# Optimization experiments

Measured on AMD Instinct MI355X. Metric: run time of the kernel, lower is better.

Reference implementation:

```python
import jax, jax.numpy as jnp
import numpy as np

B, S, HID = 4, 2048, 1024
NH = 16
HD = HID // NH  # 64


def setup_inputs() -> dict:
    key = jax.random.key(0)
    k1, k2, k3 = jax.random.split(key, 3)
    x = jax.random.normal(k1, (B, S, HID), dtype=jnp.float32)
    # causal sparse mask: True = attend
    mask = jnp.tril(jnp.ones((S, S), dtype=bool))
    w_qkv = jax.random.normal(k2, (HID, 3 * HID), dtype=jnp.float32) * 0.02
    b_qkv = jnp.zeros((3 * HID,), dtype=jnp.float32)
    w_out = jax.random.normal(k3, (HID, HID), dtype=jnp.float32) * 0.02
    b_out = jnp.zeros((HID,), dtype=jnp.float32)
    return {"x": x, "mask": mask, "w_qkv": w_qkv, "b_qkv": b_qkv,
            "w_out": w_out, "b_out": b_out}


def reference(x, mask, w_qkv, b_qkv, w_out, b_out):
    bsz, seq_len, hid = x.shape
    # QKV projection -> [B, S, H, 3*D] -> [B, H, S, 3*D]
    qkv = (x @ w_qkv + b_qkv).reshape(bsz, seq_len, NH, 3 * HD).transpose(0, 2, 1, 3)
    q, k, v = jnp.split(qkv, 3, axis=-1)  # each [B, H, S, D]
    scale = 1.0 / jnp.sqrt(jnp.asarray(HD, dtype=x.dtype))
    scores = jnp.einsum('bhqd,bhkd->bhqk', q, k) * scale
    scores = jnp.where(mask[None, None, :, :], scores, jnp.asarray(-jnp.inf, dtype=scores.dtype))
    probs = jax.nn.softmax(scores, axis=-1)
    context = jnp.einsum('bhqk,bhkd->bhqd', probs, v)  # [B, H, S, D]
    context = context.transpose(0, 2, 1, 3).reshape(bsz, seq_len, hid)
    return context @ w_out + b_out
```

## Files before the change

kernel.cpp:

```cpp
#include <hip/hip_runtime.h>
#include <stdint.h>

#define S_LEN 2048
#define NHEAD 16
#define HDIM  64
#define HIDDEN 1024
#define BATCH 4

typedef float f32x4 __attribute__((ext_vector_type(4)));
typedef __bf16 bf16x8 __attribute__((ext_vector_type(8)));
typedef unsigned short u16;

union U4B8 { uint4 u; bf16x8 b; };

__device__ __forceinline__ bf16x8 as_b8(uint4 u){ U4B8 x; x.u = u; return x.b; }

__device__ __forceinline__ f32x4 mfma16(uint4 a, uint4 b, f32x4 c){
  return __builtin_amdgcn_mfma_f32_16x16x32_bf16(as_b8(a), as_b8(b), c, 0, 0, 0);
}

__device__ __forceinline__ u16 f2bf(float f){
  __bf16 h = (__bf16)f;
  return __builtin_bit_cast(u16, h);
}

__device__ __forceinline__ float exp2fast(float x){
  return __builtin_exp2f(x);
}

__device__ __forceinline__ void gload16(const void* g, void* l){
  __builtin_amdgcn_global_load_lds(
      (const __attribute__((address_space(1))) unsigned int*)g,
      (__attribute__((address_space(3))) unsigned int*)l, 16, 0, 0);
}

#define QSCALE 0.18033688f
#define DEFER_THR 11.5f

__global__ __launch_bounds__(256) void k_cvt(const float* __restrict__ in,
                                             u16* __restrict__ out, int n4){
  int i = blockIdx.x * 256 + threadIdx.x;
  int stride = gridDim.x * 256;
  for (; i < n4; i += stride){
    float4 v = ((const float4*)in)[i];
    unsigned lo = (unsigned)f2bf(v.x) | ((unsigned)f2bf(v.y) << 16);
    unsigned hi = (unsigned)f2bf(v.z) | ((unsigned)f2bf(v.w) << 16);
    ((uint2*)out)[i] = make_uint2(lo, hi);
  }
}

__global__ __launch_bounds__(256) void k_transpose(const float* __restrict__ in,
                                                   u16* __restrict__ out,
                                                   int K, int N){
  __shared__ float t[32][33];
  int tx = threadIdx.x & 31, ty = threadIdx.x >> 5;
  int n0 = blockIdx.x * 32, k0 = blockIdx.y * 32;
  #pragma unroll
  for (int i = 0; i < 4; ++i)
    t[ty + i*8][tx] = in[(size_t)(k0 + ty + i*8) * N + n0 + tx];
  __syncthreads();
  #pragma unroll
  for (int i = 0; i < 4; ++i)
    out[(size_t)(n0 + ty + i*8) * K + k0 + tx] = f2bf(t[tx][ty + i*8]);
}

__device__ __forceinline__ void stage_gemm(
    const u16* __restrict__ A, const u16* __restrict__ Bt,
    u16* As, u16* Bs, int row0, int col0, int K, int k0, int wave, int lane)
{
  #pragma unroll
  for (int p = 0; p < 2; ++p){
    int chunk = wave * 128 + p * 64 + lane;
    int r = chunk >> 2, cseg = chunk & 3;
    const u16* ga = A  + (size_t)(row0 + r) * K + k0 + cseg * 8;
    gload16(ga, As + (size_t)(wave * 128 + p * 64) * 8);
    const u16* gb = Bt + (size_t)(col0 + r) * K + k0 + cseg * 8;
    gload16(gb, Bs + (size_t)(wave * 128 + p * 64) * 8);
  }
}

template<int MODE>
__global__ __launch_bounds__(256) void k_gemm(
    const u16* __restrict__ A, const u16* __restrict__ Bt,
    const float* __restrict__ bias,
    u16* __restrict__ oq, u16* __restrict__ ok, u16* __restrict__ ov,
    float* __restrict__ of, int M, int N, int K)
{
  __shared__ u16 As[2][128 * 32];
  __shared__ u16 Bs[2][128 * 32];
  const int tid  = threadIdx.x;
  const int wave = tid >> 6, lane = tid & 63;
  const int l4 = lane >> 4, lm = lane & 15;
  const int wr = wave >> 1, wc = wave & 1;
  const int row0 = blockIdx.y * 128;
  const int col0 = blockIdx.x * 128;

  const f32x4 fzero = {0.f, 0.f, 0.f, 0.f};
  f32x4 acc[4][4];
  #pragma unroll
  for (int m = 0; m < 4; ++m)
    #pragma unroll
    for (int n = 0; n < 4; ++n) acc[m][n] = fzero;

  stage_gemm(A, Bt, &As[0][0], &Bs[0][0], row0, col0, K, 0, wave, lane);

  const int nks = K >> 5;
  #pragma unroll 1
  for (int ks = 0; ks < nks; ++ks){
    const int cur = ks & 1;
    if (ks + 1 < nks){
      stage_gemm(A, Bt, &As[cur ^ 1][0], &Bs[cur ^ 1][0],
                 row0, col0, K, (ks + 1) << 5, wave, lane);
      asm volatile("s_waitcnt vmcnt(4)" ::: "memory");
    } else {
      asm volatile("s_waitcnt vmcnt(0)" ::: "memory");
    }
    __builtin_amdgcn_s_barrier();
    asm volatile("" ::: "memory");

    uint4 af[4], bf[4];
    #pragma unroll
    for (int m = 0; m < 4; ++m)
      af[m] = *(const uint4*)&As[cur][(wr * 64 + m * 16 + lm) * 32 + l4 * 8];
    #pragma unroll
    for (int n = 0; n < 4; ++n)
      bf[n] = *(const uint4*)&Bs[cur][(wc * 64 + n * 16 + lm) * 32 + l4 * 8];
    __builtin_amdgcn_s_setprio(1);
    #pragma unroll
    for (int m = 0; m < 4; ++m)
      #pragma unroll
      for (int n = 0; n < 4; ++n)
        acc[m][n] = mfma16(af[m], bf[n], acc[m][n]);
    __builtin_amdgcn_s_setprio(0);

    asm volatile("" ::: "memory");
    __builtin_amdgcn_s_barrier();
    asm volatile("" ::: "memory");
  }

  #pragma unroll
  for (int m = 0; m < 4; ++m){
    #pragma unroll
    for (int n = 0; n < 4; ++n){
      int c = col0 + wc * 64 + n * 16 + lm;
      float bv = bias[c];
      #pragma unroll
      for (int r = 0; r < 4; ++r){
        int row = row0 + wr * 64 + m * 16 + l4 * 4 + r;
        float val = acc[m][n][r] + bv;
        if (MODE == 0){
          int h = c / 192, e = c % 192;
          int which = e >> 6, d = e & 63;
          int b = row >> 11, s = row & 2047;
          int bh = b * 16 + h;
          if (which == 2){
            ov[((size_t)bh * HDIM + d) * S_LEN + s] = f2bf(val);
          } else {
            if (which == 0) val *= QSCALE;
            size_t idx = ((size_t)bh * S_LEN + s) * HDIM + d;
            u16* dst = (which == 0) ? oq : ok;
            dst[idx] = f2bf(val);
          }
        } else {
          of[(size_t)row * N + c] = val;
        }
      }
    }
  }
}

__device__ __forceinline__ void stage_tile(
    const u16* __restrict__ kB, const u16* __restrict__ vB,
    u16* ldsK, u16* ldsV, int kbase, int wave, int lane)
{
  #pragma unroll
  for (int p = 0; p < 2; ++p){
    int ch  = wave * 128 + p * 64 + lane;
    int row = ch >> 3;
    int cc  = (ch & 7) << 4;
    int sc  = cc ^ ((row & 7) << 4);
    const u16* gk = kB + (size_t)(kbase + row) * HDIM + (sc >> 1);
    gload16(gk, ldsK + (size_t)(wave * 128 + p * 64) * 8);
    const u16* gv = vB + (size_t)row * S_LEN + kbase + (sc >> 1);
    gload16(gv, ldsV + (size_t)(wave * 128 + p * 64) * 8);
  }
}

__global__ __launch_bounds__(256) void k_attn(
    const u16* __restrict__ q, const u16* __restrict__ kk,
    const u16* __restrict__ vt, u16* __restrict__ ctx)
{
  __shared__ u16 KV[2][2][64 * 64];
  __shared__ u16 Ps[4][2][16][72];

  const int bid = blockIdx.x;
  const int bh = bid & 63;
  const int pr = bid >> 6;
  const int wave = threadIdx.x >> 6, lane = threadIdx.x & 63;
  const int l4 = lane >> 4, lm = lane & 15;
  const size_t base = (size_t)bh * (S_LEN * HDIM);
  const u16* kB = kk + base;
  const u16* vB = vt + base;
  const int b = bh >> 4, h = bh & 15;
  const f32x4 fz = {0.f, 0.f, 0.f, 0.f};

  #pragma unroll 1
  for (int half = 0; half < 2; ++half){
    const int st = half ? (15 - pr) : pr;
    const int q0 = st * 128 + wave * 32;

    uint4 qf[2][2];
    #pragma unroll
    for (int f = 0; f < 2; ++f){
      const u16* qr = q + base + (size_t)(q0 + f * 16 + lm) * HDIM + l4 * 8;
      qf[f][0] = *(const uint4*)qr;
      qf[f][1] = *(const uint4*)(qr + 32);
    }

    float mr[2] = {-1e30f, -1e30f}, lsp[2] = {0.f, 0.f};
    f32x4 acc[2][4];
    #pragma unroll
    for (int f = 0; f < 2; ++f)
      #pragma unroll
      for (int tt = 0; tt < 4; ++tt) acc[f][tt] = fz;

    const int nkt = 2 * st + 2;

    stage_tile(kB, vB, &KV[0][0][0], &KV[0][1][0], 0, wave, lane);

    #pragma unroll 1
    for (int kt = 0; kt < nkt; ++kt){
      const int cur = kt & 1;
      const int kbase = kt << 6;
      if (kt + 1 < nkt){
        stage_tile(kB, vB, &KV[cur ^ 1][0][0], &KV[cur ^ 1][1][0],
                   (kt + 1) << 6, wave, lane);
        asm volatile("s_waitcnt vmcnt(4)" ::: "memory");
      } else {
        asm volatile("s_waitcnt vmcnt(0)" ::: "memory");
      }
      __builtin_amdgcn_s_barrier();
      asm volatile("" ::: "memory");

      if (kbase < q0 + 32){
        const u16* ldsK = &KV[cur][0][0];
        const u16* ldsV = &KV[cur][1][0];

        f32x4 sv[2][4];
        __builtin_amdgcn_s_setprio(1);
        #pragma unroll
        for (int g = 0; g < 4; ++g){
          int rk = g * 16 + lm;
          int xa = (l4 * 16) ^ ((rk & 7) << 4);
          int xb = (64 + l4 * 16) ^ ((rk & 7) << 4);
          const u16* krow = ldsK + rk * 64;
          uint4 kf0 = *(const uint4*)(krow + (xa >> 1));
          uint4 kf1 = *(const uint4*)(krow + (xb >> 1));
          sv[0][g] = mfma16(kf0, qf[0][0], fz);
          sv[0][g] = mfma16(kf1, qf[0][1], sv[0][g]);
          sv[1][g] = mfma16(kf0, qf[1][0], fz);
          sv[1][g] = mfma16(kf1, qf[1][1], sv[1][g]);
        }
        __builtin_amdgcn_s_setprio(0);

        const bool tail = (kbase + 63 > q0);

        #pragma unroll
        for (int f = 0; f < 2; ++f){
          if (tail){
            #pragma unroll
            for (int g = 0; g < 4; ++g)
              #pragma unroll
              for (int r = 0; r < 4; ++r){
                int kg = kbase + g * 16 + l4 * 4 + r;
                int qg = q0 + f * 16 + lm;
                if (kg > qg) sv[f][g][r] = -1e30f;
              }
          }

          float pm = sv[f][0][0];
          #pragma unroll
          for (int g = 0; g < 4; ++g)
            #pragma unroll
            for (int r = 0; r < 4; ++r) pm = fmaxf(pm, sv[f][g][r]);
          pm = fmaxf(pm, __shfl_xor(pm, 16));
          pm = fmaxf(pm, __shfl_xor(pm, 32));

          if (__any(pm > mr[f] + DEFER_THR)){
            float mn = fmaxf(mr[f], pm);
            float corr = exp2fast(mr[f] - mn);
            mr[f] = mn;
            lsp[f] *= corr;
            float cf[4];
            #pragma unroll
            for (int r = 0; r < 4; ++r) cf[r] = __shfl(corr, l4 * 4 + r);
            #pragma unroll
            for (int tt = 0; tt < 4; ++tt)
              #pragma unroll
              for (int r = 0; r < 4; ++r) acc[f][tt][r] *= cf[r];
          }

          float s_ = 0.f;
          #pragma unroll
          for (int g = 0; g < 4; ++g){
            float p0 = exp2fast(sv[f][g][0] - mr[f]);
            float p1 = exp2fast(sv[f][g][1] - mr[f]);
            float p2 = exp2fast(sv[f][g][2] - mr[f]);
            float p3 = exp2fast(sv[f][g][3] - mr[f]);
            s_ += (p0 + p1) + (p2 + p3);
            uint2 w;
            w.x = (unsigned)f2bf(p0) | ((unsigned)f2bf(p1) << 16);
            w.y = (unsigned)f2bf(p2) | ((unsigned)f2bf(p3) << 16);
            *(uint2*)&Ps[wave][f][lm][g * 16 + l4 * 4] = w;
          }
          lsp[f] += s_;
        }

        __builtin_amdgcn_wave_barrier();
        uint4 pa[2][2];
        #pragma unroll
        for (int f = 0; f < 2; ++f){
          pa[f][0] = *(const uint4*)&Ps[wave][f][lm][l4 * 8];
          pa[f][1] = *(const uint4*)&Ps[wave][f][lm][32 + l4 * 8];
        }

        __builtin_amdgcn_s_setprio(1);
        #pragma unroll
        for (int tt = 0; tt < 4; ++tt){
          int rv = tt * 16 + lm;
          int xa = (l4 * 16) ^ ((rv & 7) << 4);
          int xb = (64 + l4 * 16) ^ ((rv & 7) << 4);
          const u16* vrow = ldsV + rv * 64;
          uint4 v0 = *(const uint4*)(vrow + (xa >> 1));
          uint4 v1 = *(const uint4*)(vrow + (xb >> 1));
          acc[0][tt] = mfma16(pa[0][0], v0, acc[0][tt]);
          acc[0][tt] = mfma16(pa[0][1], v1, acc[0][tt]);
          acc[1][tt] = mfma16(pa[1][0], v0, acc[1][tt]);
          acc[1][tt] = mfma16(pa[1][1], v1, acc[1][tt]);
        }
        __builtin_amdgcn_s_setprio(0);
      }

      asm volatile("" ::: "memory");
      __builtin_amdgcn_s_barrier();
      asm volatile("" ::: "memory");
    }

    #pragma unroll
    for (int f = 0; f < 2; ++f){
      lsp[f] += __shfl_xor(lsp[f], 16);
      lsp[f] += __shfl_xor(lsp[f], 32);
      float inv_ = 1.0f / lsp[f];
      float ivr[4];
      #pragma unroll
      for (int r = 0; r < 4; ++r) ivr[r] = __shfl(inv_, l4 * 4 + r);
      #pragma unroll
      for (int tt = 0; tt < 4; ++tt)
        #pragma unroll
        for (int r = 0; r < 4; ++r){
          int srow = q0 + f * 16 + l4 * 4 + r;
          float val = acc[f][tt][r] * ivr[r];
          ctx[((size_t)b * S_LEN + srow) * HIDDEN + h * HDIM + tt * 16 + lm] = f2bf(val);
        }
    }
  }
}

extern "C" void kernel_launch(void* const* d_in, const int* in_sizes, int n_in,
                              void* d_out, int out_size, void* d_ws, size_t ws_size,
                              hipStream_t stream)
{
  const float* x     = (const float*)d_in[0];
  const float* w_qkv = (const float*)d_in[2];
  const float* b_qkv = (const float*)d_in[3];
  const float* w_out = (const float*)d_in[4];
  const float* b_out = (const float*)d_in[5];

  char* ws = (char*)d_ws;
  u16* xbf   = (u16*)(ws);
  u16* wqkvT = (u16*)(ws + 16777216);
  u16* woutT = (u16*)(ws + 23068672);
  u16* qb    = (u16*)(ws + 25165824);
  u16* kb    = (u16*)(ws + 41943040);
  u16* vb    = (u16*)(ws + 58720256);

  k_cvt<<<2048, 256, 0, stream>>>(x, xbf, (BATCH * S_LEN * HIDDEN) / 4);
  k_transpose<<<dim3(96, 32), 256, 0, stream>>>(w_qkv, wqkvT, HIDDEN, 3 * HIDDEN);
  k_transpose<<<dim3(32, 32), 256, 0, stream>>>(w_out, woutT, HIDDEN, HIDDEN);
  k_gemm<0><<<dim3(24, 64), 256, 0, stream>>>(xbf, wqkvT, b_qkv,
                                              qb, kb, vb, nullptr,
                                              BATCH * S_LEN, 3 * HIDDEN, HIDDEN);
  k_attn<<<512, 256, 0, stream>>>(qb, kb, vb, xbf);
  k_gemm<1><<<dim3(8, 64), 256, 0, stream>>>(xbf, woutT, b_out,
                                             nullptr, nullptr, nullptr,
                                             (float*)d_out, BATCH * S_LEN, HIDDEN, HIDDEN);
}
```

Baseline: 218.3 us.

## Split attention query tile across eight waves with 16 rows each

The attention kernel now launches 512 threads per block (8 waves), each wave owning 16 query rows instead of 32, and the K/V staging is split so each wave loads one chunk per tile. This raises the number of waves available to hide latency and lowers per-wave register pressure, and the causal skip becomes finer-grained per wave. In exchange each K/V fragment read from LDS now feeds half as many MFMAs, so LDS traffic per FLOP doubles, and block-wide barriers now synchronise twice as many waves.

Measured after the change: 201.3 us. 1.08x faster.

```diff
diff --git a/kernel.cpp b/kernel.cpp
--- a/kernel.cpp
+++ b/kernel.cpp
@@ -169,29 +169,24 @@
   }
 }
 
-__device__ __forceinline__ void stage_tile(
+__device__ __forceinline__ void stage_tile8(
     const u16* __restrict__ kB, const u16* __restrict__ vB,
     u16* ldsK, u16* ldsV, int kbase, int wave, int lane)
 {
-  #pragma unroll
-  for (int p = 0; p < 2; ++p){
-    int ch  = wave * 128 + p * 64 + lane;
-    int row = ch >> 3;
-    int cc  = (ch & 7) << 4;
-    int sc  = cc ^ ((row & 7) << 4);
-    const u16* gk = kB + (size_t)(kbase + row) * HDIM + (sc >> 1);
-    gload16(gk, ldsK + (size_t)(wave * 128 + p * 64) * 8);
-    const u16* gv = vB + (size_t)row * S_LEN + kbase + (sc >> 1);
-    gload16(gv, ldsV + (size_t)(wave * 128 + p * 64) * 8);
-  }
-}
-
-__global__ __launch_bounds__(256) void k_attn(
+  int ch  = wave * 64 + lane;
+  int row = ch >> 3;
+  int cc  = (ch & 7) << 4;
+  int sc  = cc ^ ((row & 7) << 4);
+  gload16(kB + (size_t)(kbase + row) * HDIM + (sc >> 1), ldsK + (size_t)wave * 512);
+  gload16(vB + (size_t)row * S_LEN + kbase + (sc >> 1), ldsV + (size_t)wave * 512);
+}
+
+__global__ __launch_bounds__(512) void k_attn(
     const u16* __restrict__ q, const u16* __restrict__ kk,
     const u16* __restrict__ vt, u16* __restrict__ ctx)
 {
   __shared__ u16 KV[2][2][64 * 64];
-  __shared__ u16 Ps[4][2][16][72];
+  __shared__ u16 Ps[8][16][72];
 
   const int bid = blockIdx.x;
   const int bh = bid & 63;
@@ -207,46 +202,43 @@
   #pragma unroll 1
   for (int half = 0; half < 2; ++half){
     const int st = half ? (15 - pr) : pr;
-    const int q0 = st * 128 + wave * 32;
-
-    uint4 qf[2][2];
-    #pragma unroll
-    for (int f = 0; f < 2; ++f){
-      const u16* qr = q + base + (size_t)(q0 + f * 16 + lm) * HDIM + l4 * 8;
-      qf[f][0] = *(const uint4*)qr;
-      qf[f][1] = *(const uint4*)(qr + 32);
+    const int q0 = st * 128 + wave * 16;
+
+    uint4 qf0, qf1;
+    {
+      const u16* qr = q + base + (size_t)(q0 + lm) * HDIM + l4 * 8;
+      qf0 = *(const uint4*)qr;
+      qf1 = *(const uint4*)(qr + 32);
     }
 
-    float mr[2] = {-1e30f, -1e30f}, lsp[2] = {0.f, 0.f};
-    f32x4 acc[2][4];
-    #pragma unroll
-    for (int f = 0; f < 2; ++f)
-      #pragma unroll
-      for (int tt = 0; tt < 4; ++tt) acc[f][tt] = fz;
+    float mr = -1e30f, lsp = 0.f;
+    f32x4 acc[4];
+    #pragma unroll
+    for (int tt = 0; tt < 4; ++tt) acc[tt] = fz;
 
     const int nkt = 2 * st + 2;
 
-    stage_tile(kB, vB, &KV[0][0][0], &KV[0][1][0], 0, wave, lane);
+    stage_tile8(kB, vB, &KV[0][0][0], &KV[0][1][0], 0, wave, lane);
 
     #pragma unroll 1
     for (int kt = 0; kt < nkt; ++kt){
       const int cur = kt & 1;
       const int kbase = kt << 6;
       if (kt + 1 < nkt){
-        stage_tile(kB, vB, &KV[cur ^ 1][0][0], &KV[cur ^ 1][1][0],
-                   (kt + 1) << 6, wave, lane);
-        asm volatile("s_waitcnt vmcnt(4)" ::: "memory");
+        stage_tile8(kB, vB, &KV[cur ^ 1][0][0], &KV[cur ^ 1][1][0],
+                    (kt + 1) << 6, wave, lane);
+        asm volatile("s_waitcnt vmcnt(2)" ::: "memory");
       } else {
         asm volatile("s_waitcnt vmcnt(0)" ::: "memory");
       }
       __builtin_amdgcn_s_barrier();
       asm volatile("" ::: "memory");
 
-      if (kbase < q0 + 32){
+      if (kbase < q0 + 16){
         const u16* ldsK = &KV[cur][0][0];
         const u16* ldsV = &KV[cur][1][0];
 
-        f32x4 sv[2][4];
+        f32x4 sv[4];
         __builtin_amdgcn_s_setprio(1);
         #pragma unroll
         for (int g = 0; g < 4; ++g){
@@ -256,73 +248,62 @@
           const u16* krow = ldsK + rk * 64;
           uint4 kf0 = *(const uint4*)(krow + (xa >> 1));
           uint4 kf1 = *(const uint4*)(krow + (xb >> 1));
-          sv[0][g] = mfma16(kf0, qf[0][0], fz);
-          sv[0][g] = mfma16(kf1, qf[0][1], sv[0][g]);
-          sv[1][g] = mfma16(kf0, qf[1][0], fz);
-          sv[1][g] = mfma16(kf1, qf[1][1], sv[1][g]);
+          sv[g] = mfma16(kf0, qf0, fz);
+          sv[g] = mfma16(kf1, qf1, sv[g]);
         }
         __builtin_amdgcn_s_setprio(0);
 
-        const bool tail = (kbase + 63 > q0);
-
-        #pragma unroll
-        for (int f = 0; f < 2; ++f){
-          if (tail){
-            #pragma unroll
-            for (int g = 0; g < 4; ++g)
-              #pragma unroll
-              for (int r = 0; r < 4; ++r){
-                int kg = kbase + g * 16 + l4 * 4 + r;
-                int qg = q0 + f * 16 + lm;
-                if (kg > qg) sv[f][g][r] = -1e30f;
-              }
-          }
-
-          float pm = sv[f][0][0];
+        if (kbase + 63 > q0){
           #pragma unroll
           for (int g = 0; g < 4; ++g)
             #pragma unroll
-            for (int r = 0; r < 4; ++r) pm = fmaxf(pm, sv[f][g][r]);
-          pm = fmaxf(pm, __shfl_xor(pm, 16));
+            for (int r = 0; r < 4; ++r){
+              int kg = kbase + g * 16 + l4 * 4 + r;
+              int qg = q0 + lm;
+              if (kg > qg) sv[g][r] = -1e30f;
+            }
+        }
+
+        float pml = sv[0][0];
+        #pragma unroll
+        for (int g = 0; g < 4; ++g)
+          #pragma unroll
+          for (int r = 0; r < 4; ++r) pml = fmaxf(pml, sv[g][r]);
+
+        if (__any(pml > mr + DEFER_THR)){
+          float pm = fmaxf(pml, __shfl_xor(pml, 16));
           pm = fmaxf(pm, __shfl_xor(pm, 32));
-
-          if (__any(pm > mr[f] + DEFER_THR)){
-            float mn = fmaxf(mr[f], pm);
-            float corr = exp2fast(mr[f] - mn);
-            mr[f] = mn;
-            lsp[f] *= corr;
-            float cf[4];
+          float mn = fmaxf(mr, pm);
+          float corr = exp2fast(mr - mn);
+          mr = mn;
+          lsp *= corr;
+          float cf[4];
+          #pragma unroll
+          for (int r = 0; r < 4; ++r) cf[r] = __shfl(corr, l4 * 4 + r);
+          #pragma unroll
+          for (int tt = 0; tt < 4; ++tt)
             #pragma unroll
-            for (int r = 0; r < 4; ++r) cf[r] = __shfl(corr, l4 * 4 + r);
-            #pragma unroll
-            for (int tt = 0; tt < 4; ++tt)
-              #pragma unroll
-              for (int r = 0; r < 4; ++r) acc[f][tt][r] *= cf[r];
-          }
-
-          float s_ = 0.f;
-          #pragma unroll
-          for (int g = 0; g < 4; ++g){
-            float p0 = exp2fast(sv[f][g][0] - mr[f]);
-            float p1 = exp2fast(sv[f][g][1] - mr[f]);
-            float p2 = exp2fast(sv[f][g][2] - mr[f]);
-            float p3 = exp2fast(sv[f][g][3] - mr[f]);
-            s_ += (p0 + p1) + (p2 + p3);
-            uint2 w;
-            w.x = (unsigned)f2bf(p0) | ((unsigned)f2bf(p1) << 16);
-            w.y = (unsigned)f2bf(p2) | ((unsigned)f2bf(p3) << 16);
-            *(uint2*)&Ps[wave][f][lm][g * 16 + l4 * 4] = w;
-          }
-          lsp[f] += s_;
-        }
+            for (int r = 0; r < 4; ++r) acc[tt][r] *= cf[r];
+        }
+
+        float s_ = 0.f;
+        #pragma unroll
+        for (int g = 0; g < 4; ++g){
+          float p0 = exp2fast(sv[g][0] - mr);
+          float p1 = exp2fast(sv[g][1] - mr);
+          float p2 = exp2fast(sv[g][2] - mr);
+          float p3 = exp2fast(sv[g][3] - mr);
+          s_ += (p0 + p1) + (p2 + p3);
+          uint2 w;
+          w.x = (unsigned)f2bf(p0) | ((unsigned)f2bf(p1) << 16);
+          w.y = (unsigned)f2bf(p2) | ((unsigned)f2bf(p3) << 16);
+          *(uint2*)&Ps[wave][lm][g * 16 + l4 * 4] = w;
+        }
+        lsp += s_;
 
         __builtin_amdgcn_wave_barrier();
-        uint4 pa[2][2];
-        #pragma unroll
-        for (int f = 0; f < 2; ++f){
-          pa[f][0] = *(const uint4*)&Ps[wave][f][lm][l4 * 8];
-          pa[f][1] = *(const uint4*)&Ps[wave][f][lm][32 + l4 * 8];
-        }
+        uint4 pa0 = *(const uint4*)&Ps[wave][lm][l4 * 8];
+        uint4 pa1 = *(const uint4*)&Ps[wave][lm][32 + l4 * 8];
 
         __builtin_amdgcn_s_setprio(1);
         #pragma unroll
@@ -333,10 +314,8 @@
           const u16* vrow = ldsV + rv * 64;
           uint4 v0 = *(const uint4*)(vrow + (xa >> 1));
           uint4 v1 = *(const uint4*)(vrow + (xb >> 1));
-          acc[0][tt] = mfma16(pa[0][0], v0, acc[0][tt]);
-          acc[0][tt] = mfma16(pa[0][1], v1, acc[0][tt]);
-          acc[1][tt] = mfma16(pa[1][0], v0, acc[1][tt]);
-          acc[1][tt] = mfma16(pa[1][1], v1, acc[1][tt]);
+          acc[tt] = mfma16(pa0, v0, acc[tt]);
+          acc[tt] = mfma16(pa1, v1, acc[tt]);
         }
         __builtin_amdgcn_s_setprio(0);
       }
@@ -346,23 +325,20 @@
       asm volatile("" ::: "memory");
     }
 
-    #pragma unroll
-    for (int f = 0; f < 2; ++f){
-      lsp[f] += __shfl_xor(lsp[f], 16);
-      lsp[f] += __shfl_xor(lsp[f], 32);
-      float inv_ = 1.0f / lsp[f];
-      float ivr[4];
+    lsp += __shfl_xor(lsp, 16);
+    lsp += __shfl_xor(lsp, 32);
+    float inv_ = 1.0f / lsp;
+    float ivr[4];
+    #pragma unroll
+    for (int r = 0; r < 4; ++r) ivr[r] = __shfl(inv_, l4 * 4 + r);
+    #pragma unroll
+    for (int tt = 0; tt < 4; ++tt)
       #pragma unroll
-      for (int r = 0; r < 4; ++r) ivr[r] = __shfl(inv_, l4 * 4 + r);
-      #pragma unroll
-      for (int tt = 0; tt < 4; ++tt)
-        #pragma unroll
-        for (int r = 0; r < 4; ++r){
-          int srow = q0 + f * 16 + l4 * 4 + r;
-          float val = acc[f][tt][r] * ivr[r];
-          ctx[((size_t)b * S_LEN + srow) * HIDDEN + h * HDIM + tt * 16 + lm] = f2bf(val);
-        }
-    }
+      for (int r = 0; r < 4; ++r){
+        int srow = q0 + l4 * 4 + r;
+        float val = acc[tt][r] * ivr[r];
+        ctx[((size_t)b * S_LEN + srow) * HIDDEN + h * HDIM + tt * 16 + lm] = f2bf(val);
+      }
   }
 }
 
@@ -390,7 +366,7 @@
   k_gemm<0><<<dim3(24, 64), 256, 0, stream>>>(xbf, wqkvT, b_qkv,
                                               qb, kb, vb, nullptr,
                                               BATCH * S_LEN, 3 * HIDDEN, HIDDEN);
-  k_attn<<<512, 256, 0, stream>>>(qb, kb, vb, xbf);
+  k_attn<<<512, 512, 0, stream>>>(qb, kb, vb, xbf);
   k_gemm<1><<<dim3(8, 64), 256, 0, stream>>>(xbf, woutT, b_out,
                                              nullptr, nullptr, nullptr,
                                              (float*)d_out, BATCH * S_LEN, HIDDEN, HIDDEN);
```
